# Optimization experiments

Measured on AMD Instinct MI355X. Metric: run time of the kernel, lower is better.

The kernel has to match this reference:

```python
import jax, jax.numpy as jnp
import numpy as np

NUM_EXPERTS = 8
TOP_K = 2
D = 512
F = 2048
B, L = 4, 1024


def setup_inputs() -> dict:
    key = jax.random.key(0)
    ks = jax.random.split(key, 5)
    std = D ** -0.5
    return {
        "x": jax.random.normal(ks[0], (B, L, D), jnp.float32),
        "gate_w": jax.random.normal(ks[1], (NUM_EXPERTS, D), jnp.float32) * std,
        "w1": jax.random.normal(ks[2], (NUM_EXPERTS, F, D), jnp.float32) * std,
        "w2": jax.random.normal(ks[3], (NUM_EXPERTS, D, F), jnp.float32) * (F ** -0.5),
        "w3": jax.random.normal(ks[4], (NUM_EXPERTS, F, D), jnp.float32) * std,
    }


def reference(x, gate_w, w1, w2, w3):
    b, l, d = x.shape
    xf = x.reshape(-1, d)                      # [T, D]
    T = xf.shape[0]
    router_logits = xf @ gate_w.T              # [T, E]
    # top-k routing in float32 (as in original), softmax over selected logits
    topk_w, topk_idx = jax.lax.top_k(router_logits.astype(jnp.float32), TOP_K)
    topk_w = jax.nn.softmax(topk_w, axis=-1).astype(x.dtype)  # [T, K]
    # combine weights per (token, expert): scatter top-k weights into dense [T, E]
    cw = jnp.zeros((T, NUM_EXPERTS), x.dtype)
    cw = cw.at[jnp.arange(T)[:, None], topk_idx].add(topk_w)
    # per-expert gated FFN (SiLU(x w1^T) * (x w3^T)) w2^T, batched over experts
    h = jax.nn.silu(jnp.einsum('td,efd->etf', xf, w1)) * jnp.einsum('td,efd->etf', xf, w3)
    y = jnp.einsum('etf,edf->etd', h, w2)      # [E, T, D]
    out = jnp.einsum('te,etd->td', cw, y)      # weighted combine
    return out.reshape(b, l, d), router_logits
```

## Files before the change

kernel.cpp:

```cpp
#include <hip/hip_runtime.h>

#define TTOK 4096
#define NEXP 8
#define DDIM 512
#define FDIM 2048
#define HROWS 8576

typedef __attribute__((ext_vector_type(8))) short short8;
typedef __attribute__((ext_vector_type(4))) float floatx4;

__device__ __forceinline__ ushort f2b(float f) {
  unsigned u = __float_as_uint(f);
  u += 0x7fffu + ((u >> 16) & 1u);
  return (ushort)(u >> 16);
}

__device__ __forceinline__ void load16(void* lds, const void* g) {
  __builtin_amdgcn_global_load_lds(
      (const __attribute__((address_space(1))) unsigned int*)g,
      (__attribute__((address_space(3))) unsigned int*)lds, 16, 0, 0);
}


__global__ __launch_bounds__(256) void k_logits(
    const float* __restrict__ x, const float* __restrict__ gw,
    float* __restrict__ logits, int* __restrict__ tok_e,
    float2* __restrict__ tok_w)
{
  const int lane = threadIdx.x & 63;
  const int t = blockIdx.x * 4 + (threadIdx.x >> 6);
  float xv[8];
#pragma unroll
  for (int i = 0; i < 8; ++i) xv[i] = x[(size_t)t * DDIM + lane + 64 * i];
  float lg[8];
#pragma unroll
  for (int e = 0; e < 8; ++e) {
    float a = 0.f;
#pragma unroll
    for (int i = 0; i < 8; ++i) a += xv[i] * gw[e * DDIM + lane + 64 * i];
#pragma unroll
    for (int s = 32; s; s >>= 1) a += __shfl_xor(a, s, 64);
    lg[e] = a;
  }
  if (lane < 8) logits[(size_t)t * 8 + lane] = lg[lane];
  if (lane == 0) {
    int i0 = 0; float v0 = lg[0];
#pragma unroll
    for (int e = 1; e < 8; ++e) { if (lg[e] > v0) { v0 = lg[e]; i0 = e; } }
    int i1 = -1; float v1 = -3.4e38f;
#pragma unroll
    for (int e = 0; e < 8; ++e) { if (e != i0 && lg[e] > v1) { v1 = lg[e]; i1 = e; } }
    float ex = expf(v1 - v0);
    float inv = 1.f / (1.f + ex);
    tok_e[t] = i0 | (i1 << 4);
    tok_w[t] = make_float2(inv, ex * inv);
  }
}

__global__ __launch_bounds__(1024) void k_build(
    const int* __restrict__ tok_e, const float2* __restrict__ tok_w,
    int* __restrict__ counts, int* __restrict__ lists, float* __restrict__ wts)
{
  const int e = blockIdx.x;
  const int tid = threadIdx.x;
  const int lane = tid & 63, wid = tid >> 6;
  __shared__ int wcnt[16];
  __shared__ int sbase;
  if (tid == 0) sbase = 0;
  __syncthreads();

  for (int c = 0; c < TTOK; c += 1024) {
    int t = c + tid;
    int pe = tok_e[t];
    bool m0 = (pe & 15) == e;
    bool m1 = ((pe >> 4) & 15) == e;
    bool m = m0 || m1;
    unsigned long long b = __ballot(m);
    int lpre = __popcll(b & ((1ull << lane) - 1ull));
    if (lane == 0) wcnt[wid] = __popcll(b);
    __syncthreads();
    int woff = 0;
#pragma unroll
    for (int i = 0; i < 16; ++i) if (i < wid) woff += wcnt[i];
    if (m) {
      float2 w = tok_w[t];
      int pos = sbase + woff + lpre;
      lists[e * TTOK + pos] = t;
      wts[e * TTOK + pos] = m0 ? w.x : w.y;
    }
    __syncthreads();
    if (tid == 0) {
      int s = 0;
#pragma unroll
      for (int i = 0; i < 16; ++i) s += wcnt[i];
      sbase += s;
    }
    __syncthreads();
  }
  if (tid == 0) counts[e] = sbase;
}

__global__ __launch_bounds__(256) void k_gather(
    const float* __restrict__ x, const int* __restrict__ counts,
    const int* __restrict__ lists, ushort* __restrict__ Xg)
{
  int pp[9];
  pp[0] = 0;
#pragma unroll
  for (int i = 0; i < 8; ++i) pp[i + 1] = pp[i] + ((counts[i] + 31) & ~31);
  int gid = blockIdx.x * 256 + threadIdx.x;
  int gr = gid >> 6, dg = gid & 63;
  if (gr >= pp[8]) return;
  int e = 0;
  while (e < 7 && gr >= pp[e + 1]) ++e;
  int p = gr - pp[e];
  size_t dst = ((size_t)(gr >> 4) * 16 + (dg >> 2)) * 512
             + ((gr & 15) + 16 * (dg & 3)) * 8;
  short8 o = (short8)0;
  if (p < counts[e]) {
    int t = lists[e * TTOK + p];
    const float* s = x + (size_t)t * DDIM + dg * 8;
    float4 a = *(const float4*)s;
    float4 b = *(const float4*)(s + 4);
    o[0] = f2b(a.x); o[1] = f2b(a.y); o[2] = f2b(a.z); o[3] = f2b(a.w);
    o[4] = f2b(b.x); o[5] = f2b(b.y); o[6] = f2b(b.z); o[7] = f2b(b.w);
  }
  *(short8*)&Xg[dst] = o;
}

__global__ __launch_bounds__(256) void k_cvtAll(
    const float* __restrict__ w1, ushort* __restrict__ w1t,
    const float* __restrict__ w3, ushort* __restrict__ w3t,
    const float* __restrict__ w2, ushort* __restrict__ w2t)
{
  __shared__ ushort sm[4096];
  int bid = blockIdx.x;
  const float* src; ushort* dst; int C, cbShift;
  if (bid < 2048)      { src = w1; dst = w1t; C = 512;  cbShift = 2; }
  else if (bid < 4096) { src = w3; dst = w3t; C = 512;  cbShift = 2; bid -= 2048; }
  else                 { src = w2; dst = w2t; C = 2048; cbShift = 4; bid -= 4096; }
  const int tid = threadIdx.x;
  const int r0 = (bid >> cbShift) * 32;
  const int c0 = (bid & ((1 << cbShift) - 1)) * 128;
  const int KT = C >> 5;
#pragma unroll
  for (int i = 0; i < 4; ++i) {
    int j = i * 1024 + tid * 4;
    int lr = j >> 7, lc = j & 127;
    float4 v = *(const float4*)&src[(size_t)(r0 + lr) * C + c0 + lc];
    ushort4 b = { f2b(v.x), f2b(v.y), f2b(v.z), f2b(v.w) };
    int ord = (lr >> 4) * 4 + (lc >> 5);
    int slot = (lr & 15) + 16 * ((lc >> 3) & 3);
    *(ushort4*)&sm[(ord * 64 + slot) * 8 + (lc & 7)] = b;
  }
  __syncthreads();
  const size_t tb0 = ((size_t)(r0 >> 4) * KT + (c0 >> 5)) * 512;
#pragma unroll
  for (int rt = 0; rt < 2; ++rt)
    *(short8*)&dst[tb0 + (size_t)rt * KT * 512 + tid * 8] =
        *(const short8*)&sm[rt * 2048 + tid * 8];
}

__global__ __launch_bounds__(512) void k_ffn1(
    const ushort* __restrict__ Xg, const ushort* __restrict__ w1t,
    const ushort* __restrict__ w3t, const int* __restrict__ counts,
    ushort* __restrict__ H)
{
  const int bid = blockIdx.x;
  const int widx = (bid & 7) * 512 + (bid >> 3);
  const int mt = widx & 31, e = (widx >> 5) & 7, ft = widx >> 8;
  const int ne = counts[e];
  const int m0 = mt * 128;
  if (m0 >= ne) return;
  const int f0 = ft * 128;
  int hb = 0;
#pragma unroll
  for (int i = 0; i < 7; ++i) if (i < e) hb += (counts[i] + 31) & ~31;
  const int tid = threadIdx.x;
  const int wid = tid >> 6, lane = tid & 63;
  const int wm = wid >> 2, wn = wid & 3;
  const int lr = lane & 15, lgp = lane >> 4;

  __shared__ ushort Xls[2][4096], W1ls[2][4096], W3ls[2][4096];

  const int rtX0 = (hb + m0) >> 4;
  const ushort* sx = Xg  + ((size_t)(rtX0 + wid) * 16) * 512 + lane * 8;
  const ushort* s1 = w1t + ((size_t)(e * 128 + (f0 >> 4) + wid) * 16) * 512 + lane * 8;
  const ushort* s3 = w3t + ((size_t)(e * 128 + (f0 >> 4) + wid) * 16) * 512 + lane * 8;

#define FFN1_STAGE(B)                                                       \
  { load16((char*)&Xls[B][0]  + wid * 1024, sx);                            \
    load16((char*)&W1ls[B][0] + wid * 1024, s1);                            \
    load16((char*)&W3ls[B][0] + wid * 1024, s3);                            \
    sx += 512; s1 += 512; s3 += 512; }

#define FFN1_COMPUTE(B)                                                     \
  { short8 af[4], b1[2], b3[2];                                             \
    _Pragma("unroll")                                                       \
    for (int mf = 0; mf < 4; ++mf)                                          \
      af[mf] = *(const short8*)&Xls[B][(wm * 4 + mf) * 512 + lane * 8];     \
    _Pragma("unroll")                                                       \
    for (int nf = 0; nf < 2; ++nf) {                                        \
      b1[nf] = *(const short8*)&W1ls[B][(wn * 2 + nf) * 512 + lane * 8];    \
      b3[nf] = *(const short8*)&W3ls[B][(wn * 2 + nf) * 512 + lane * 8];    \
    }                                                                       \
    _Pragma("unroll")                                                       \
    for (int mf = 0; mf < 4; ++mf)                                          \
      _Pragma("unroll")                                                     \
      for (int nf = 0; nf < 2; ++nf) {                                      \
        acc1[mf][nf] = __builtin_amdgcn_mfma_f32_16x16x32_bf16(             \
            af[mf], b1[nf], acc1[mf][nf], 0, 0, 0);                         \
        acc3[mf][nf] = __builtin_amdgcn_mfma_f32_16x16x32_bf16(             \
            af[mf], b3[nf], acc3[mf][nf], 0, 0, 0);                         \
      } }

  floatx4 acc1[4][2], acc3[4][2];
#pragma unroll
  for (int a = 0; a < 4; ++a)
#pragma unroll
    for (int b = 0; b < 2; ++b) { acc1[a][b] = (floatx4)0.f; acc3[a][b] = (floatx4)0.f; }

  FFN1_STAGE(0);
  __syncthreads();

  for (int t = 0; t < 16; t += 2) {
    if (t + 1 < 16) FFN1_STAGE(1);
    FFN1_COMPUTE(0);
    __syncthreads();
    if (t + 2 < 16) FFN1_STAGE(0);
    FFN1_COMPUTE(1);
    __syncthreads();
  }

#pragma unroll
  for (int mf = 0; mf < 4; ++mf) {
    const int rtOut = rtX0 + wm * 4 + mf;
#pragma unroll
    for (int nf = 0; nf < 2; ++nf) {
      const int kt = (f0 >> 5) + wn;
      const int slotc = (nf * 2 + (lr >> 3)) & 3;
      size_t base = ((size_t)rtOut * 64 + kt) * 512 + 16 * slotc * 8 + (lr & 7);
      floatx4 v1 = acc1[mf][nf], v3 = acc3[mf][nf];
#pragma unroll
      for (int j = 0; j < 4; ++j) {
        int p = m0 + wm * 64 + mf * 16 + lgp * 4 + j;
        if (p < ne) {
          float h1 = v1[j], h3 = v3[j];
          float sig = 1.f / (1.f + __expf(-h1));
          H[base + (size_t)(lgp * 4 + j) * 8] = f2b(h1 * sig * h3);
        }
      }
    }
  }
#undef FFN1_STAGE
#undef FFN1_COMPUTE
}

__global__ __launch_bounds__(512) void k_ffn2(
    const ushort* __restrict__ Ht, const ushort* __restrict__ w2t,
    const int* __restrict__ counts, const int* __restrict__ lists,
    const float* __restrict__ wts, float* __restrict__ out)
{
  const int bid = blockIdx.x;
  const int widx = (bid & 7) * 256 + (bid >> 3);
  const int mt = widx & 31, e = (widx >> 5) & 7;
  const int rest = widx >> 8;
  const int dt = rest & 3, ks = rest >> 2;
  const int ne = counts[e];
  const int m0 = mt * 128;
  if (m0 >= ne) return;
  const int d0 = dt * 128;
  int hb = 0;
#pragma unroll
  for (int i = 0; i < 7; ++i) if (i < e) hb += (counts[i] + 31) & ~31;
  const int tid = threadIdx.x;
  const int wid = tid >> 6, lane = tid & 63;
  const int wm = wid >> 2, wn = wid & 3;
  const int lr = lane & 15, lgp = lane >> 4;

  __shared__ ushort Hls[2][8192], W2ls[2][8192];
  __shared__ int toks[128];
  __shared__ float twt[128];

  if (tid < 128) {
    int p = m0 + tid;
    bool v = p < ne;
    toks[tid] = v ? lists[e * TTOK + p] : 0;
    twt[tid] = v ? wts[e * TTOK + p] : 0.f;
  }

  const int rtH0 = (hb + m0) >> 4;
  const int kb = ks * 32;
  const ushort* sh = Ht  + ((size_t)(rtH0 + wid) * 64 + kb) * 512 + lane * 8;
  const ushort* sw = w2t + ((size_t)(e * 32 + (d0 >> 4) + wid) * 64 + kb) * 512 + lane * 8;

#define FFN2_STAGE(B)                                                      \
  { load16((char*)&Hls[B][0]  + (wid * 2) * 1024, sh);                     \
    load16((char*)&Hls[B][0]  + (wid * 2 + 1) * 1024, sh + 512);           \
    load16((char*)&W2ls[B][0] + (wid * 2) * 1024, sw);                     \
    load16((char*)&W2ls[B][0] + (wid * 2 + 1) * 1024, sw + 512);           \
    sh += 1024; sw += 1024; }

#define FFN2_COMPUTE(B)                                                    \
  { _Pragma("unroll")                                                      \
    for (int kk = 0; kk < 2; ++kk) {                                       \
      short8 af[4], bf[2];                                                 \
      _Pragma("unroll")                                                    \
      for (int mf = 0; mf < 4; ++mf)                                       \
        af[mf] = *(const short8*)&Hls[B][((wm * 4 + mf) * 2 + kk) * 512 + lane * 8]; \
      _Pragma("unroll")                                                    \
      for (int nf = 0; nf < 2; ++nf)                                       \
        bf[nf] = *(const short8*)&W2ls[B][((wn * 2 + nf) * 2 + kk) * 512 + lane * 8]; \
      _Pragma("unroll")                                                    \
      for (int mf = 0; mf < 4; ++mf)                                       \
        _Pragma("unroll")                                                  \
        for (int nf = 0; nf < 2; ++nf)                                     \
          acc[mf][nf] = __builtin_amdgcn_mfma_f32_16x16x32_bf16(           \
              af[mf], bf[nf], acc[mf][nf], 0, 0, 0);                       \
    } }

  floatx4 acc[4][2];
#pragma unroll
  for (int a = 0; a < 4; ++a)
#pragma unroll
    for (int b = 0; b < 2; ++b) acc[a][b] = (floatx4)0.f;

  FFN2_STAGE(0);
  __syncthreads();

  for (int t = 0; t < 16; t += 2) {
    if (t + 1 < 16) FFN2_STAGE(1);
    FFN2_COMPUTE(0);
    __syncthreads();
    if (t + 2 < 16) FFN2_STAGE(0);
    FFN2_COMPUTE(1);
    __syncthreads();
  }

#pragma unroll
  for (int mf = 0; mf < 4; ++mf) {
#pragma unroll
    for (int j = 0; j < 4; ++j) {
      int rloc = wm * 64 + mf * 16 + lgp * 4 + j;
      int p = m0 + rloc;
      if (p < ne) {
        int t = toks[rloc];
        float w = twt[rloc];
#pragma unroll
        for (int nf = 0; nf < 2; ++nf) {
          int d = d0 + wn * 32 + nf * 16 + lr;
          atomicAdd(&out[(size_t)t * DDIM + d], w * acc[mf][nf][j]);
        }
      }
    }
  }
#undef FFN2_STAGE
#undef FFN2_COMPUTE
}

extern "C" void kernel_launch(void* const* d_in, const int* in_sizes, int n_in,
                              void* d_out, int out_size, void* d_ws, size_t ws_size,
                              hipStream_t stream) {
  const float* x  = (const float*)d_in[0];
  const float* gw = (const float*)d_in[1];
  const float* w1 = (const float*)d_in[2];
  const float* w2 = (const float*)d_in[3];
  const float* w3 = (const float*)d_in[4];
  float* out = (float*)d_out;
  float* logits = out + (size_t)TTOK * DDIM;

  int* counts = (int*)d_ws;
  int* tok_e  = counts + 16;
  float2* tok_w = (float2*)(tok_e + TTOK);
  int* lists  = (int*)(tok_w + TTOK);
  float* wts  = (float*)(lists + NEXP * TTOK);
  ushort* w1t = (ushort*)(wts + NEXP * TTOK);
  ushort* w3t = w1t + (size_t)NEXP * FDIM * DDIM;
  ushort* w2t = w3t + (size_t)NEXP * FDIM * DDIM;
  ushort* Xg  = w2t + (size_t)NEXP * DDIM * FDIM;
  ushort* H   = Xg + (size_t)HROWS * DDIM;

  hipMemsetAsync(d_out, 0, (size_t)TTOK * DDIM * sizeof(float), stream);

  k_logits<<<TTOK / 4, 256, 0, stream>>>(x, gw, logits, tok_e, tok_w);
  k_build<<<NEXP, 1024, 0, stream>>>(tok_e, tok_w, counts, lists, wts);
  k_gather<<<(8448 * 64) / 256, 256, 0, stream>>>(x, counts, lists, Xg);

  k_cvtAll<<<6144, 256, 0, stream>>>(w1, w1t, w3, w3t, w2, w2t);

  k_ffn1<<<4096, 512, 0, stream>>>(Xg, w1t, w3t, counts, H);
  k_ffn2<<<2048, 512, 0, stream>>>(H, w2t, counts, lists, wts, out);
}
```

Baseline: 157.2 us.

## Fold weight conversion into logits and ffn1 launches; use vmcnt-based pipelining barriers

The standalone weight-conversion kernel is removed. w1/w3 conversion now runs as extra blocks in the logits kernel and w2 conversion as extra blocks appended to ffn1, which cuts launches and lets conversion overlap with routing and FFN1 work. The FFN1 and FFN2 main loops replace __syncthreads with explicit s_waitcnt vmcnt counts plus raw s_barrier and sched_barrier, so the next stage's loads stay in flight while the current stage computes. The risks are the hand-tuned vmcnt values and w2 conversion blocks competing with ffn1 tiles for compute units.

Measured after the change: 146.2 us. -7.0%, faster.

```diff
diff --git a/kernel.cpp b/kernel.cpp
--- a/kernel.cpp
+++ b/kernel.cpp
@@ -9,6 +9,9 @@
 typedef __attribute__((ext_vector_type(8))) short short8;
 typedef __attribute__((ext_vector_type(4))) float floatx4;
 
+#define BAR()  __builtin_amdgcn_s_barrier()
+#define SBAR() __builtin_amdgcn_sched_barrier(0)
+
 __device__ __forceinline__ ushort f2b(float f) {
   unsigned u = __float_as_uint(f);
   u += 0x7fffu + ((u >> 16) & 1u);
@@ -22,39 +25,68 @@
 }
 
 
-__global__ __launch_bounds__(256) void k_logits(
+__global__ __launch_bounds__(256) void k_front(
     const float* __restrict__ x, const float* __restrict__ gw,
     float* __restrict__ logits, int* __restrict__ tok_e,
-    float2* __restrict__ tok_w)
+    float2* __restrict__ tok_w,
+    const float* __restrict__ w1, ushort* __restrict__ w1t,
+    const float* __restrict__ w3, ushort* __restrict__ w3t)
 {
-  const int lane = threadIdx.x & 63;
-  const int t = blockIdx.x * 4 + (threadIdx.x >> 6);
-  float xv[8];
-#pragma unroll
-  for (int i = 0; i < 8; ++i) xv[i] = x[(size_t)t * DDIM + lane + 64 * i];
-  float lg[8];
-#pragma unroll
-  for (int e = 0; e < 8; ++e) {
-    float a = 0.f;
-#pragma unroll
-    for (int i = 0; i < 8; ++i) a += xv[i] * gw[e * DDIM + lane + 64 * i];
-#pragma unroll
-    for (int s = 32; s; s >>= 1) a += __shfl_xor(a, s, 64);
-    lg[e] = a;
-  }
-  if (lane < 8) logits[(size_t)t * 8 + lane] = lg[lane];
-  if (lane == 0) {
-    int i0 = 0; float v0 = lg[0];
-#pragma unroll
-    for (int e = 1; e < 8; ++e) { if (lg[e] > v0) { v0 = lg[e]; i0 = e; } }
-    int i1 = -1; float v1 = -3.4e38f;
-#pragma unroll
-    for (int e = 0; e < 8; ++e) { if (e != i0 && lg[e] > v1) { v1 = lg[e]; i1 = e; } }
-    float ex = expf(v1 - v0);
-    float inv = 1.f / (1.f + ex);
-    tok_e[t] = i0 | (i1 << 4);
-    tok_w[t] = make_float2(inv, ex * inv);
-  }
+  __shared__ ushort sm[4096];
+  const int tid = threadIdx.x;
+  if (blockIdx.x < TTOK / 4) {
+    const int lane = tid & 63;
+    const int t = blockIdx.x * 4 + (tid >> 6);
+    float xv[8];
+#pragma unroll
+    for (int i = 0; i < 8; ++i) xv[i] = x[(size_t)t * DDIM + lane + 64 * i];
+    float lg[8];
+#pragma unroll
+    for (int e = 0; e < 8; ++e) {
+      float a = 0.f;
+#pragma unroll
+      for (int i = 0; i < 8; ++i) a += xv[i] * gw[e * DDIM + lane + 64 * i];
+#pragma unroll
+      for (int s = 32; s; s >>= 1) a += __shfl_xor(a, s, 64);
+      lg[e] = a;
+    }
+    if (lane < 8) logits[(size_t)t * 8 + lane] = lg[lane];
+    if (lane == 0) {
+      int i0 = 0; float v0 = lg[0];
+#pragma unroll
+      for (int e = 1; e < 8; ++e) { if (lg[e] > v0) { v0 = lg[e]; i0 = e; } }
+      int i1 = -1; float v1 = -3.4e38f;
+#pragma unroll
+      for (int e = 0; e < 8; ++e) { if (e != i0 && lg[e] > v1) { v1 = lg[e]; i1 = e; } }
+      float ex = expf(v1 - v0);
+      float inv = 1.f / (1.f + ex);
+      tok_e[t] = i0 | (i1 << 4);
+      tok_w[t] = make_float2(inv, ex * inv);
+    }
+    return;
+  }
+  int bid = blockIdx.x - TTOK / 4;
+  const float* src = (bid < 2048) ? w1 : w3;
+  ushort* dst = (bid < 2048) ? w1t : w3t;
+  if (bid >= 2048) bid -= 2048;
+  const int r0 = (bid >> 2) * 32;
+  const int c0 = (bid & 3) * 128;
+#pragma unroll
+  for (int i = 0; i < 4; ++i) {
+    int j = i * 1024 + tid * 4;
+    int lr = j >> 7, lc = j & 127;
+    float4 v = *(const float4*)&src[(size_t)(r0 + lr) * 512 + c0 + lc];
+    ushort4 b = { f2b(v.x), f2b(v.y), f2b(v.z), f2b(v.w) };
+    int ord = (lr >> 4) * 4 + (lc >> 5);
+    int slot = (lr & 15) + 16 * ((lc >> 3) & 3);
+    *(ushort4*)&sm[(ord * 64 + slot) * 8 + (lc & 7)] = b;
+  }
+  __syncthreads();
+  const size_t tb0 = ((size_t)(r0 >> 4) * 16 + (c0 >> 5)) * 512;
+#pragma unroll
+  for (int rt = 0; rt < 2; ++rt)
+    *(short8*)&dst[tb0 + (size_t)rt * 16 * 512 + tid * 8] =
+        *(const short8*)&sm[rt * 2048 + tid * 8];
 }
 
 __global__ __launch_bounds__(1024) void k_build(
@@ -128,44 +160,38 @@
   *(short8*)&Xg[dst] = o;
 }
 
-__global__ __launch_bounds__(256) void k_cvtAll(
-    const float* __restrict__ w1, ushort* __restrict__ w1t,
-    const float* __restrict__ w3, ushort* __restrict__ w3t,
-    const float* __restrict__ w2, ushort* __restrict__ w2t)
-{
-  __shared__ ushort sm[4096];
-  int bid = blockIdx.x;
-  const float* src; ushort* dst; int C, cbShift;
-  if (bid < 2048)      { src = w1; dst = w1t; C = 512;  cbShift = 2; }
-  else if (bid < 4096) { src = w3; dst = w3t; C = 512;  cbShift = 2; bid -= 2048; }
-  else                 { src = w2; dst = w2t; C = 2048; cbShift = 4; bid -= 4096; }
-  const int tid = threadIdx.x;
-  const int r0 = (bid >> cbShift) * 32;
-  const int c0 = (bid & ((1 << cbShift) - 1)) * 128;
-  const int KT = C >> 5;
-#pragma unroll
-  for (int i = 0; i < 4; ++i) {
-    int j = i * 1024 + tid * 4;
-    int lr = j >> 7, lc = j & 127;
-    float4 v = *(const float4*)&src[(size_t)(r0 + lr) * C + c0 + lc];
-    ushort4 b = { f2b(v.x), f2b(v.y), f2b(v.z), f2b(v.w) };
-    int ord = (lr >> 4) * 4 + (lc >> 5);
-    int slot = (lr & 15) + 16 * ((lc >> 3) & 3);
-    *(ushort4*)&sm[(ord * 64 + slot) * 8 + (lc & 7)] = b;
-  }
-  __syncthreads();
-  const size_t tb0 = ((size_t)(r0 >> 4) * KT + (c0 >> 5)) * 512;
-#pragma unroll
-  for (int rt = 0; rt < 2; ++rt)
-    *(short8*)&dst[tb0 + (size_t)rt * KT * 512 + tid * 8] =
-        *(const short8*)&sm[rt * 2048 + tid * 8];
-}
-
 __global__ __launch_bounds__(512) void k_ffn1(
     const ushort* __restrict__ Xg, const ushort* __restrict__ w1t,
     const ushort* __restrict__ w3t, const int* __restrict__ counts,
-    ushort* __restrict__ H)
+    ushort* __restrict__ H,
+    const float* __restrict__ w2, ushort* __restrict__ w2t)
 {
+  __shared__ ushort Xls[2][4096], W1ls[2][4096], W3ls[2][4096];
+  const int tid = threadIdx.x;
+
+  if (blockIdx.x >= 4096) {
+    int bid = blockIdx.x - 4096;
+    ushort* sm = &Xls[0][0];
+    const int r0 = (bid >> 4) * 32;
+    const int c0 = (bid & 15) * 128;
+#pragma unroll
+    for (int i = 0; i < 2; ++i) {
+      int j = i * 2048 + tid * 4;
+      int lr = j >> 7, lc = j & 127;
+      float4 v = *(const float4*)&w2[(size_t)(r0 + lr) * 2048 + c0 + lc];
+      ushort4 b = { f2b(v.x), f2b(v.y), f2b(v.z), f2b(v.w) };
+      int ord = (lr >> 4) * 4 + (lc >> 5);
+      int slot = (lr & 15) + 16 * ((lc >> 3) & 3);
+      *(ushort4*)&sm[(ord * 64 + slot) * 8 + (lc & 7)] = b;
+    }
+    __syncthreads();
+    const size_t tb0 = ((size_t)(r0 >> 4) * 64 + (c0 >> 5)) * 512;
+    int rt = tid >> 8, s = tid & 255;
+    *(short8*)&w2t[tb0 + (size_t)rt * 64 * 512 + s * 8] =
+        *(const short8*)&sm[rt * 2048 + s * 8];
+    return;
+  }
+
   const int bid = blockIdx.x;
   const int widx = (bid & 7) * 512 + (bid >> 3);
   const int mt = widx & 31, e = (widx >> 5) & 7, ft = widx >> 8;
@@ -176,12 +202,9 @@
   int hb = 0;
 #pragma unroll
   for (int i = 0; i < 7; ++i) if (i < e) hb += (counts[i] + 31) & ~31;
-  const int tid = threadIdx.x;
   const int wid = tid >> 6, lane = tid & 63;
   const int wm = wid >> 2, wn = wid & 3;
   const int lr = lane & 15, lgp = lane >> 4;
-
-  __shared__ ushort Xls[2][4096], W1ls[2][4096], W3ls[2][4096];
 
   const int rtX0 = (hb + m0) >> 4;
   const ushort* sx = Xg  + ((size_t)(rtX0 + wid) * 16) * 512 + lane * 8;
@@ -221,15 +244,21 @@
     for (int b = 0; b < 2; ++b) { acc1[a][b] = (floatx4)0.f; acc3[a][b] = (floatx4)0.f; }
 
   FFN1_STAGE(0);
-  __syncthreads();
-
   for (int t = 0; t < 16; t += 2) {
-    if (t + 1 < 16) FFN1_STAGE(1);
+    FFN1_STAGE(1);
+    asm volatile("s_waitcnt vmcnt(3)" ::: "memory");
+    BAR(); SBAR();
     FFN1_COMPUTE(0);
-    __syncthreads();
-    if (t + 2 < 16) FFN1_STAGE(0);
+    SBAR(); BAR();
+    if (t + 2 < 16) {
+      FFN1_STAGE(0);
+      asm volatile("s_waitcnt vmcnt(3)" ::: "memory");
+    } else {
+      asm volatile("s_waitcnt vmcnt(0)" ::: "memory");
+    }
+    BAR(); SBAR();
     FFN1_COMPUTE(1);
-    __syncthreads();
+    SBAR(); BAR();
   }
 
 #pragma unroll
@@ -326,15 +355,21 @@
     for (int b = 0; b < 2; ++b) acc[a][b] = (floatx4)0.f;
 
   FFN2_STAGE(0);
-  __syncthreads();
-
   for (int t = 0; t < 16; t += 2) {
-    if (t + 1 < 16) FFN2_STAGE(1);
+    FFN2_STAGE(1);
+    asm volatile("s_waitcnt vmcnt(4)" ::: "memory");
+    BAR(); SBAR();
     FFN2_COMPUTE(0);
-    __syncthreads();
-    if (t + 2 < 16) FFN2_STAGE(0);
+    SBAR(); BAR();
+    if (t + 2 < 16) {
+      FFN2_STAGE(0);
+      asm volatile("s_waitcnt vmcnt(4)" ::: "memory");
+    } else {
+      asm volatile("s_waitcnt vmcnt(0)" ::: "memory");
+    }
+    BAR(); SBAR();
     FFN2_COMPUTE(1);
-    __syncthreads();
+    SBAR(); BAR();
   }
 
 #pragma unroll
@@ -382,12 +417,11 @@
 
   hipMemsetAsync(d_out, 0, (size_t)TTOK * DDIM * sizeof(float), stream);
 
-  k_logits<<<TTOK / 4, 256, 0, stream>>>(x, gw, logits, tok_e, tok_w);
+  k_front<<<TTOK / 4 + 4096, 256, 0, stream>>>(x, gw, logits, tok_e, tok_w,
+                                               w1, w1t, w3, w3t);
   k_build<<<NEXP, 1024, 0, stream>>>(tok_e, tok_w, counts, lists, wts);
   k_gather<<<(8448 * 64) / 256, 256, 0, stream>>>(x, counts, lists, Xg);
 
-  k_cvtAll<<<6144, 256, 0, stream>>>(w1, w1t, w3, w3t, w2, w2t);
-
-  k_ffn1<<<4096, 512, 0, stream>>>(Xg, w1t, w3t, counts, H);
+  k_ffn1<<<4096 + 2048, 512, 0, stream>>>(Xg, w1t, w3t, counts, H, w2, w2t);
   k_ffn2<<<2048, 512, 0, stream>>>(H, w2t, counts, lists, wts, out);
 }
```
